# Kernel tuning notes

Measured on AMD Instinct MI355X. Metric: run time of the kernel, lower is better.

## Reference

```python
import jax, jax.numpy as jnp
import numpy as np

CH = 256
RED = 4
CQK = CH // RED

def _conv(x, w, b):
    # x: [B,C,H,W], w: [O,I,3,3], b: [O]; SAME padding (pad=1)
    y = jax.lax.conv_general_dilated(
        x, w, window_strides=(1, 1), padding=((1, 1), (1, 1)),
        dimension_numbers=('NCHW', 'OIHW', 'NCHW'))
    return y + b[None, :, None, None]

def setup_inputs() -> dict:
    key = jax.random.key(0)
    ks = jax.random.split(key, 7)
    x = jax.random.normal(ks[0], (4, CH, 64, 64), dtype=jnp.float32)
    fan_in = CH * 9
    s = 1.0 / np.sqrt(fan_in)
    q_w = jax.random.uniform(ks[1], (CQK, CH, 3, 3), jnp.float32, -s, s)
    q_b = jax.random.uniform(ks[2], (CQK,), jnp.float32, -s, s)
    k_w = jax.random.uniform(ks[3], (CQK, CH, 3, 3), jnp.float32, -s, s)
    k_b = jax.random.uniform(ks[4], (CQK,), jnp.float32, -s, s)
    v_w = jax.random.uniform(ks[5], (CH, CH, 3, 3), jnp.float32, -s, s)
    v_b = jax.random.uniform(ks[6], (CH,), jnp.float32, -s, s)
    return {"x": x, "q_w": q_w, "q_b": q_b, "k_w": k_w, "k_b": k_b,
            "v_w": v_w, "v_b": v_b}

def reference(x, q_w, q_b, k_w, k_b, v_w, v_b):
    b, c, h, w = x.shape
    hw = h * w
    scale = CQK ** (-0.5)
    q = _conv(x, q_w, q_b).reshape(b, CQK, hw)   # [B, Cqk, HW]
    k = _conv(x, k_w, k_b).reshape(b, CQK, hw)   # [B, Cqk, HW]
    v = _conv(x, v_w, v_b).reshape(b, c, hw)     # [B, C,   HW]
    # attn[b,i,j] = sum_d q[b,d,i] * k[b,d,j]
    attn = jnp.einsum('bdi,bdj->bij', q, k) * scale
    attn = jax.nn.softmax(attn, axis=-1)         # [B, HW, HW]
    # out[b,c,i] = sum_j v[b,c,j] * attn[b,i,j]  (torch: bmm(v, attn^T))
    out = jnp.einsum('bcj,bij->bci', v, attn).reshape(b, c, h, w)
    return out
```

## Files before the change

kernel.cpp:

```cpp
#include <hip/hip_runtime.h>
#include <stdint.h>

typedef unsigned short u16;
typedef short short8 __attribute__((ext_vector_type(8)));
typedef short short4v __attribute__((ext_vector_type(4)));
typedef float float4v __attribute__((ext_vector_type(4)));
typedef uint32_t uint2v __attribute__((ext_vector_type(2)));

#define HW 4096
#define SCL 0.18033688011112042f

#define GLOAD_LDS(g, l) __builtin_amdgcn_global_load_lds( \
    (const __attribute__((address_space(1))) void*)(g),   \
    (__attribute__((address_space(3))) void*)(l), 16, 0, 0)

static __device__ __forceinline__ u16 f2bf(float f) {
  union { float f; uint32_t u; } v; v.f = f;
  uint32_t r = v.u + 0x7fffu + ((v.u >> 16) & 1u);
  return (u16)(r >> 16);
}
static __device__ __forceinline__ uint32_t f2bf_u32(float f) {
  union { float f; uint32_t u; } v; v.f = f;
  return (v.u + 0x8000u) >> 16;
}

__global__ __launch_bounds__(256) void k_xt(const float* __restrict__ x, u16* __restrict__ Xtp) {
  __shared__ float t[32][33];
  const int b = blockIdx.z, c0 = blockIdx.y * 32, p0 = blockIdx.x * 32;
  const int tid = threadIdx.x;
  const int l8 = tid >> 5, lp = tid & 31;
#pragma unroll
  for (int i = 0; i < 4; i++) {
    int c = l8 + i * 8;
    t[c][lp] = x[(size_t)(b * 256 + c0 + c) * HW + p0 + lp];
  }
  __syncthreads();
#pragma unroll
  for (int i = 0; i < 4; i++) {
    int p = l8 + i * 8;
    int pp = p0 + p;
    int y = pp >> 6, xx = pp & 63;
    Xtp[((size_t)(b * 66 + y + 1) * 66 + (xx + 1)) * 256 + c0 + lp] = f2bf(t[lp][p]);
  }
}

__global__ __launch_bounds__(256) void k_wprep(const float* __restrict__ qw, const float* __restrict__ qb,
    const float* __restrict__ kw, const float* __restrict__ kb,
    const float* __restrict__ vw, const float* __restrict__ vb,
    u16* __restrict__ Wt, float* __restrict__ bcat) {
  int tid = blockIdx.x * 256 + threadIdx.x;
  if (tid < 9 * 384 * 256) {
    int ci = tid & 255;
    int n = (tid >> 8) % 384;
    int off = tid / (384 * 256);
    float val;
    if (n < 64)       val = qw[(size_t)n * 2304 + ci * 9 + off];
    else if (n < 128) val = kw[(size_t)(n - 64) * 2304 + ci * 9 + off];
    else              val = vw[(size_t)(n - 128) * 2304 + ci * 9 + off];
    Wt[tid] = f2bf(val);
  }
  if (tid < 384) bcat[tid] = (tid < 64) ? qb[tid] : (tid < 128) ? kb[tid - 64] : vb[tid - 128];
}

__global__ __launch_bounds__(256) void k_conv(const u16* __restrict__ Xtp,
    const u16* __restrict__ Wt, const float* __restrict__ bcat,
    u16* __restrict__ Qt, u16* __restrict__ Kt, u16* __restrict__ Vcf) {
  __shared__ __align__(16) u16 Als[2][128 * 64];
  __shared__ __align__(16) u16 Bls[2][64 * 64];
  const int tid = threadIdx.x;
  const int b = blockIdx.z, ct = blockIdx.y;
  const int p0 = blockIdx.x * 128, n0 = ct * 64;
  const int w = tid >> 6, lane = tid & 63, l16 = lane & 15, quad = lane >> 4;

  const int lr = lane >> 3, lcx = (lane & 7) ^ lr;
  const u16* ag[4];
#pragma unroll
  for (int g = 0; g < 4; g++) {
    const int pos = p0 + w * 32 + g * 8 + lr;
    const int py = pos >> 6, px = pos & 63;
    ag[g] = Xtp + ((size_t)(b * 66 + py) * 66 + px) * 256 + lcx * 8;
  }
  const u16* bg[2];
#pragma unroll
  for (int g = 0; g < 2; g++)
    bg[g] = Wt + (size_t)(n0 + w * 16 + g * 8 + lr) * 256 + lcx * 8;

  const int rx = l16 & 7;

  float4v acc[2][4];
  const float4v zz = {0.f, 0.f, 0.f, 0.f};
#pragma unroll
  for (int i = 0; i < 2; i++)
#pragma unroll
    for (int j = 0; j < 4; j++) acc[i][j] = zz;

#pragma unroll
  for (int g = 0; g < 4; g++) GLOAD_LDS(ag[g], &Als[0][(w * 32 + g * 8) * 64]);
#pragma unroll
  for (int g = 0; g < 2; g++) GLOAD_LDS(bg[g], &Bls[0][(w * 16 + g * 8) * 64]);
  __syncthreads();

  for (int ks = 0; ks < 36; ks++) {
    const int buf = ks & 1;
    if (ks + 1 < 36) {
      const int ksn = ks + 1, tap = ksn >> 2, cg = (ksn & 3) * 64;
      const int dy = (tap * 11) >> 5, dx = tap - dy * 3;
      const int aoff = (dy * 66 + dx) * 256 + cg;
      const size_t boff = (size_t)tap * 98304 + cg;
#pragma unroll
      for (int g = 0; g < 4; g++) GLOAD_LDS(ag[g] + aoff, &Als[buf ^ 1][(w * 32 + g * 8) * 64]);
#pragma unroll
      for (int g = 0; g < 2; g++) GLOAD_LDS(bg[g] + boff, &Bls[buf ^ 1][(w * 16 + g * 8) * 64]);
    }

    short8 af[2][2], bfv[4][2];
#pragma unroll
    for (int mt = 0; mt < 2; mt++)
#pragma unroll
      for (int kk = 0; kk < 2; kk++)
        af[mt][kk] = *(const short8*)&Als[buf][(w * 32 + mt * 16 + l16) * 64 + (((kk * 4 + quad) ^ rx) * 8)];
#pragma unroll
    for (int nt = 0; nt < 4; nt++)
#pragma unroll
      for (int kk = 0; kk < 2; kk++)
        bfv[nt][kk] = *(const short8*)&Bls[buf][(nt * 16 + l16) * 64 + (((kk * 4 + quad) ^ rx) * 8)];

    if (ct < 2) {
#pragma unroll
      for (int mt = 0; mt < 2; mt++)
#pragma unroll
        for (int nt = 0; nt < 4; nt++)
#pragma unroll
          for (int kk = 0; kk < 2; kk++)
            acc[mt][nt] = __builtin_amdgcn_mfma_f32_16x16x32_bf16(bfv[nt][kk], af[mt][kk], acc[mt][nt], 0, 0, 0);
    } else {
#pragma unroll
      for (int mt = 0; mt < 2; mt++)
#pragma unroll
        for (int nt = 0; nt < 4; nt++)
#pragma unroll
          for (int kk = 0; kk < 2; kk++)
            acc[mt][nt] = __builtin_amdgcn_mfma_f32_16x16x32_bf16(af[mt][kk], bfv[nt][kk], acc[mt][nt], 0, 0, 0);
    }
    __syncthreads();
  }

  if (ct < 2) {
    u16* base = (ct == 0) ? Qt : Kt;
#pragma unroll
    for (int mt = 0; mt < 2; mt++) {
      const int p = p0 + w * 32 + mt * 16 + l16;
#pragma unroll
      for (int nt = 0; nt < 4; nt++) {
        const int nb = nt * 16 + quad * 4;
        short4v o;
#pragma unroll
        for (int r = 0; r < 4; r++) o[r] = (short)f2bf(acc[mt][nt][r] + bcat[ct * 64 + nb + r]);
        *(short4v*)(base + (size_t)(b * HW + p) * 64 + nb) = o;
      }
    }
  } else {
#pragma unroll
    for (int mt = 0; mt < 2; mt++) {
      const int pb = p0 + w * 32 + mt * 16 + quad * 4;
#pragma unroll
      for (int nt = 0; nt < 4; nt++) {
        const int cl = nt * 16 + l16;
        const int gc = (ct - 2) * 64 + cl;
        const float bias = bcat[ct * 64 + cl];
        short4v o;
#pragma unroll
        for (int r = 0; r < 4; r++) o[r] = (short)f2bf(acc[mt][nt][r] + bias);
        *(short4v*)(Vcf + (size_t)(b * 256 + gc) * HW + pb) = o;
      }
    }
  }
}

__global__ __launch_bounds__(256, 2) void k_attn(const u16* __restrict__ Qt,
    const u16* __restrict__ Kt, const u16* __restrict__ Vcf, float* __restrict__ out) {
  __shared__ __align__(16) u16 Kls[2][64 * 64];
  __shared__ __align__(16) u16 Vls[2][128 * 64];
  __shared__ __align__(16) u16 Pls[4][16][66];
  const int tid = threadIdx.x;
  const int b = blockIdx.y, ib = blockIdx.x * 64, cs = blockIdx.z * 128;
  const int w = tid >> 6, lane = tid & 63, l16 = lane & 15, quad = lane >> 4;
  const int i0 = ib + w * 16;

  const u16* Kb = Kt + (size_t)b * HW * 64;
  const u16* Vb = Vcf + ((size_t)b * 256 + cs) * HW;

  const int lr = lane >> 3, lcx = (lane & 7) ^ lr;
  const size_t koff = (size_t)lr * 128 + (size_t)lcx * 16;
  const size_t voff = (size_t)lr * (HW * 2) + (size_t)lcx * 16;

  const int kA = (quad ^ (l16 & 7)) * 8;
  const int rowu = l16 * 64;

  short8 qf[2];
  {
    const u16* qp = Qt + (size_t)(b * HW + i0 + l16) * 64 + quad * 8;
    qf[0] = *(const short8*)qp;
    qf[1] = *(const short8*)(qp + 32);
  }

  float4v of[8];
  const float4v zz = {0.f, 0.f, 0.f, 0.f};
#pragma unroll
  for (int nt = 0; nt < 8; nt++) of[nt] = zz;
  float lsum = 0.f;

  {
    const char* kg = (const char*)Kb + (size_t)(w * 16) * 128;
    const char* vg = (const char*)Vb + (size_t)(w * 32) * (HW * 2);
#pragma unroll
    for (int g = 0; g < 2; g++)
      GLOAD_LDS(kg + g * 1024 + koff, &Kls[0][(w * 16 + g * 8) * 64]);
#pragma unroll
    for (int g = 0; g < 4; g++)
      GLOAD_LDS(vg + (size_t)g * 8 * (HW * 2) + voff, &Vls[0][(w * 32 + g * 8) * 64]);
  }
  __syncthreads();

  for (int jt = 0; jt < 64; jt++) {
    const int buf = jt & 1;
    {
      const int jn = ((jt + 1) & 63) * 64;
      const char* kg = (const char*)Kb + (size_t)(jn + w * 16) * 128;
      const char* vg = (const char*)Vb + (size_t)(w * 32) * (HW * 2) + (size_t)jn * 2;
#pragma unroll
      for (int g = 0; g < 2; g++)
        GLOAD_LDS(kg + g * 1024 + koff, &Kls[buf ^ 1][(w * 16 + g * 8) * 64]);
#pragma unroll
      for (int g = 0; g < 4; g++)
        GLOAD_LDS(vg + (size_t)g * 8 * (HW * 2) + voff, &Vls[buf ^ 1][(w * 32 + g * 8) * 64]);
    }

    float4v sf[4];
#pragma unroll
    for (int nt = 0; nt < 4; nt++) sf[nt] = zz;
#pragma unroll
    for (int nt = 0; nt < 4; nt++) {
      short8 k0 = *(const short8*)&Kls[buf][nt * 1024 + rowu + kA];
      short8 k1 = *(const short8*)&Kls[buf][nt * 1024 + rowu + (kA ^ 32)];
      sf[nt] = __builtin_amdgcn_mfma_f32_16x16x32_bf16(k0, qf[0], sf[nt], 0, 0, 0);
      sf[nt] = __builtin_amdgcn_mfma_f32_16x16x32_bf16(k1, qf[1], sf[nt], 0, 0, 0);
    }

    float rs = 0.f;
#pragma unroll
    for (int nt = 0; nt < 4; nt++) {
      float p0 = exp2f(sf[nt][0] * SCL);
      float p1 = exp2f(sf[nt][1] * SCL);
      float p2 = exp2f(sf[nt][2] * SCL);
      float p3 = exp2f(sf[nt][3] * SCL);
      rs += (p0 + p1) + (p2 + p3);
      uint2v pd;
      pd[0] = f2bf_u32(p0) | (f2bf_u32(p1) << 16);
      pd[1] = f2bf_u32(p2) | (f2bf_u32(p3) << 16);
      *(uint2v*)&Pls[w][l16][nt * 16 + quad * 4] = pd;
    }
    rs += __shfl_xor(rs, 16);
    rs += __shfl_xor(rs, 32);
    lsum += rs;

    __builtin_amdgcn_sched_barrier(0);
    __builtin_amdgcn_s_waitcnt(0xC07F);
    __builtin_amdgcn_sched_barrier(0);

#pragma unroll
    for (int kk = 0; kk < 2; kk++) {
      short8 pfr = *(const short8*)&Pls[w][l16][kk * 32 + quad * 8];
      const int vcol = kk ? (kA ^ 32) : kA;
#pragma unroll
      for (int nt = 0; nt < 8; nt++) {
        short8 vf = *(const short8*)&Vls[buf][nt * 1024 + rowu + vcol];
        of[nt] = __builtin_amdgcn_mfma_f32_16x16x32_bf16(vf, pfr, of[nt], 0, 0, 0);
      }
    }
    __syncthreads();
  }

  const float inv = 1.0f / lsum;
#pragma unroll
  for (int nt = 0; nt < 8; nt++)
#pragma unroll
    for (int r = 0; r < 4; r++)
      out[(size_t)(b * 256 + cs + nt * 16 + quad * 4 + r) * HW + i0 + l16] = of[nt][r] * inv;
}

extern "C" void kernel_launch(void* const* d_in, const int* in_sizes, int n_in,
                              void* d_out, int out_size, void* d_ws, size_t ws_size,
                              hipStream_t stream) {
  const float* x  = (const float*)d_in[0];
  const float* qw = (const float*)d_in[1];
  const float* qb = (const float*)d_in[2];
  const float* kw = (const float*)d_in[3];
  const float* kb = (const float*)d_in[4];
  const float* vw = (const float*)d_in[5];
  const float* vb = (const float*)d_in[6];
  float* out = (float*)d_out;
  char* ws = (char*)d_ws;
  u16*   Xtp = (u16*)(ws);
  u16*   Wt  = (u16*)(ws + 8921088);
  float* bc  = (float*)(ws + 10690560);
  u16*   Qt  = (u16*)(ws + 10692096);
  u16*   Kt  = (u16*)(ws + 12789248);
  u16*   Vcf = (u16*)(ws + 14886400);

  hipMemsetAsync(Xtp, 0, 8921088, stream);
  k_xt  <<<dim3(128, 8, 4), 256, 0, stream>>>(x, Xtp);
  k_wprep<<<3456, 256, 0, stream>>>(qw, qb, kw, kb, vw, vb, Wt, bc);
  k_conv<<<dim3(32, 6, 4), 256, 0, stream>>>(Xtp, Wt, bc, Qt, Kt, Vcf);
  k_attn<<<dim3(64, 4, 2), 256, 0, stream>>>(Qt, Kt, Vcf, out);
}
```

Measured before the change: 212.3 us.

## Fold softmax scale into Q, split P staging, pack transpose stores, raise occupancy

```diff
diff --git a/kernel.cpp b/kernel.cpp
--- a/kernel.cpp
+++ b/kernel.cpp
@@ -19,28 +19,30 @@
   uint32_t r = v.u + 0x7fffu + ((v.u >> 16) & 1u);
   return (u16)(r >> 16);
 }
-static __device__ __forceinline__ uint32_t f2bf_u32(float f) {
+static __device__ __forceinline__ uint32_t bfbits(float f) {
   union { float f; uint32_t u; } v; v.f = f;
-  return (v.u + 0x8000u) >> 16;
+  return v.u + 0x8000u;
 }
 
 __global__ __launch_bounds__(256) void k_xt(const float* __restrict__ x, u16* __restrict__ Xtp) {
-  __shared__ float t[32][33];
-  const int b = blockIdx.z, c0 = blockIdx.y * 32, p0 = blockIdx.x * 32;
+  __shared__ float t[64][33];
+  const int b = blockIdx.z, c0 = blockIdx.y * 64, p0 = blockIdx.x * 32;
   const int tid = threadIdx.x;
-  const int l8 = tid >> 5, lp = tid & 31;
-#pragma unroll
-  for (int i = 0; i < 4; i++) {
-    int c = l8 + i * 8;
+  const int row = tid >> 5, lp = tid & 31;
+#pragma unroll
+  for (int i = 0; i < 8; i++) {
+    int c = i * 8 + row;
     t[c][lp] = x[(size_t)(b * 256 + c0 + c) * HW + p0 + lp];
   }
   __syncthreads();
 #pragma unroll
-  for (int i = 0; i < 4; i++) {
-    int p = l8 + i * 8;
+  for (int j = 0; j < 4; j++) {
+    int p = j * 8 + row;
     int pp = p0 + p;
     int y = pp >> 6, xx = pp & 63;
-    Xtp[((size_t)(b * 66 + y + 1) * 66 + (xx + 1)) * 256 + c0 + lp] = f2bf(t[lp][p]);
+    uint32_t lo = f2bf(t[lp * 2][p]);
+    uint32_t hi = f2bf(t[lp * 2 + 1][p]);
+    *(uint32_t*)&Xtp[((size_t)(b * 66 + y + 1) * 66 + (xx + 1)) * 256 + c0 + lp * 2] = lo | (hi << 16);
   }
 }
 
@@ -147,6 +149,7 @@
 
   if (ct < 2) {
     u16* base = (ct == 0) ? Qt : Kt;
+    const float sc = (ct == 0) ? SCL : 1.0f;
 #pragma unroll
     for (int mt = 0; mt < 2; mt++) {
       const int p = p0 + w * 32 + mt * 16 + l16;
@@ -155,7 +158,7 @@
         const int nb = nt * 16 + quad * 4;
         short4v o;
 #pragma unroll
-        for (int r = 0; r < 4; r++) o[r] = (short)f2bf(acc[mt][nt][r] + bcat[ct * 64 + nb + r]);
+        for (int r = 0; r < 4; r++) o[r] = (short)f2bf((acc[mt][nt][r] + bcat[ct * 64 + nb + r]) * sc);
         *(short4v*)(base + (size_t)(b * HW + p) * 64 + nb) = o;
       }
     }
@@ -177,11 +180,11 @@
   }
 }
 
-__global__ __launch_bounds__(256, 2) void k_attn(const u16* __restrict__ Qt,
+__global__ __launch_bounds__(256, 3) void k_attn(const u16* __restrict__ Qt,
     const u16* __restrict__ Kt, const u16* __restrict__ Vcf, float* __restrict__ out) {
   __shared__ __align__(16) u16 Kls[2][64 * 64];
   __shared__ __align__(16) u16 Vls[2][128 * 64];
-  __shared__ __align__(16) u16 Pls[4][16][66];
+  __shared__ __align__(16) u16 Pls[4][16][40];
   const int tid = threadIdx.x;
   const int b = blockIdx.y, ib = blockIdx.x * 64, cs = blockIdx.z * 128;
   const int w = tid >> 6, lane = tid & 63, l16 = lane & 15, quad = lane >> 4;
@@ -249,35 +252,57 @@
 
     float rs = 0.f;
 #pragma unroll
-    for (int nt = 0; nt < 4; nt++) {
-      float p0 = exp2f(sf[nt][0] * SCL);
-      float p1 = exp2f(sf[nt][1] * SCL);
-      float p2 = exp2f(sf[nt][2] * SCL);
-      float p3 = exp2f(sf[nt][3] * SCL);
+    for (int nt = 0; nt < 2; nt++) {
+      float p0 = exp2f(sf[nt][0]);
+      float p1 = exp2f(sf[nt][1]);
+      float p2 = exp2f(sf[nt][2]);
+      float p3 = exp2f(sf[nt][3]);
       rs += (p0 + p1) + (p2 + p3);
       uint2v pd;
-      pd[0] = f2bf_u32(p0) | (f2bf_u32(p1) << 16);
-      pd[1] = f2bf_u32(p2) | (f2bf_u32(p3) << 16);
+      pd[0] = __builtin_amdgcn_perm(bfbits(p1), bfbits(p0), 0x07060302u);
+      pd[1] = __builtin_amdgcn_perm(bfbits(p3), bfbits(p2), 0x07060302u);
       *(uint2v*)&Pls[w][l16][nt * 16 + quad * 4] = pd;
     }
+    __builtin_amdgcn_sched_barrier(0);
+    __builtin_amdgcn_s_waitcnt(0xC07F);
+    __builtin_amdgcn_sched_barrier(0);
+    {
+      short8 pfr = *(const short8*)&Pls[w][l16][quad * 8];
+#pragma unroll
+      for (int nt = 0; nt < 8; nt++) {
+        short8 vf = *(const short8*)&Vls[buf][nt * 1024 + rowu + kA];
+        of[nt] = __builtin_amdgcn_mfma_f32_16x16x32_bf16(vf, pfr, of[nt], 0, 0, 0);
+      }
+    }
+
+#pragma unroll
+    for (int nt = 2; nt < 4; nt++) {
+      float p0 = exp2f(sf[nt][0]);
+      float p1 = exp2f(sf[nt][1]);
+      float p2 = exp2f(sf[nt][2]);
+      float p3 = exp2f(sf[nt][3]);
+      rs += (p0 + p1) + (p2 + p3);
+      uint2v pd;
+      pd[0] = __builtin_amdgcn_perm(bfbits(p1), bfbits(p0), 0x07060302u);
+      pd[1] = __builtin_amdgcn_perm(bfbits(p3), bfbits(p2), 0x07060302u);
+      *(uint2v*)&Pls[w][l16][(nt - 2) * 16 + quad * 4] = pd;
+    }
+    __builtin_amdgcn_sched_barrier(0);
+    __builtin_amdgcn_s_waitcnt(0xC07F);
+    __builtin_amdgcn_sched_barrier(0);
+    {
+      short8 pfr = *(const short8*)&Pls[w][l16][quad * 8];
+#pragma unroll
+      for (int nt = 0; nt < 8; nt++) {
+        short8 vf = *(const short8*)&Vls[buf][nt * 1024 + rowu + (kA ^ 32)];
+        of[nt] = __builtin_amdgcn_mfma_f32_16x16x32_bf16(vf, pfr, of[nt], 0, 0, 0);
+      }
+    }
+
     rs += __shfl_xor(rs, 16);
     rs += __shfl_xor(rs, 32);
     lsum += rs;
 
-    __builtin_amdgcn_sched_barrier(0);
-    __builtin_amdgcn_s_waitcnt(0xC07F);
-    __builtin_amdgcn_sched_barrier(0);
-
-#pragma unroll
-    for (int kk = 0; kk < 2; kk++) {
-      short8 pfr = *(const short8*)&Pls[w][l16][kk * 32 + quad * 8];
-      const int vcol = kk ? (kA ^ 32) : kA;
-#pragma unroll
-      for (int nt = 0; nt < 8; nt++) {
-        short8 vf = *(const short8*)&Vls[buf][nt * 1024 + rowu + vcol];
-        of[nt] = __builtin_amdgcn_mfma_f32_16x16x32_bf16(vf, pfr, of[nt], 0, 0, 0);
-      }
-    }
     __syncthreads();
   }
 
@@ -309,7 +334,7 @@
   u16*   Vcf = (u16*)(ws + 14886400);
 
   hipMemsetAsync(Xtp, 0, 8921088, stream);
-  k_xt  <<<dim3(128, 8, 4), 256, 0, stream>>>(x, Xtp);
+  k_xt  <<<dim3(128, 4, 4), 256, 0, stream>>>(x, Xtp);
   k_wprep<<<3456, 256, 0, stream>>>(qw, qb, kw, kb, vw, vb, Wt, bc);
   k_conv<<<dim3(32, 6, 4), 256, 0, stream>>>(Xtp, Wt, bc, Qt, Kt, Vcf);
   k_attn<<<dim3(64, 4, 2), 256, 0, stream>>>(Qt, Kt, Vcf, out);
```

Result: slower. 217.3 us (+2.4%).
